# Kernel tuning notes

Measured on AMD Instinct MI355X. Metric: run time of the kernel, lower is better.

The kernel has to match this reference:

```python
import jax, jax.numpy as jnp
import numpy as np

B, C, H, W = 16, 256, 96, 96
PLANES = 64            # inplanes * ratio = 256 * 0.25
HEADS = 4
EPS = 1e-5             # BatchNorm eps


def setup_inputs() -> dict:
    key = jax.random.key(0)
    ks = jax.random.split(key, 8)
    HW = H * W
    G = HW // HEADS    # group size of the grouped 1x1 conv over spatial-positions-as-channels
    return {
        "x": jax.random.normal(ks[0], (B, C, H, W), jnp.float32),
        # input_conv: Conv1x1(C->PLANES) -> BN -> ReLU -> Conv1x1(PLANES->C)
        "w1": jax.random.normal(ks[1], (PLANES, C), jnp.float32) * (1.0 / np.sqrt(C)),
        "b1": jax.random.normal(ks[2], (PLANES,), jnp.float32) * 0.01,
        "gamma": jnp.ones((PLANES,), jnp.float32),
        "beta": jnp.zeros((PLANES,), jnp.float32),
        "mean": jnp.zeros((PLANES,), jnp.float32),
        "var": jnp.ones((PLANES,), jnp.float32),
        "w2": jax.random.normal(ks[3], (C, PLANES), jnp.float32) * (1.0 / np.sqrt(PLANES)),
        "b2": jax.random.normal(ks[4], (C,), jnp.float32) * 0.01,
        # conv_mask: Conv2d(HW, HEADS, k=1, groups=HEADS) -> weight [HEADS, G], bias [HEADS]
        "wm": jax.random.normal(ks[5], (HEADS, G), jnp.float32) * (1.0 / np.sqrt(G)),
        "bm": jax.random.normal(ks[6], (HEADS,), jnp.float32) * 0.01,
    }


def reference(x, w1, b1, gamma, beta, mean, var, w2, b2, wm, bm):
    Bx, Cx, Hx, Wx = x.shape
    G = (Hx * Wx) // HEADS
    # ---- input_conv: 1x1 conv -> BN (inference) -> ReLU -> 1x1 conv ----
    h = jnp.einsum('bchw,pc->bphw', x, w1) + b1[None, :, None, None]
    scale = (gamma / jnp.sqrt(var + EPS))[None, :, None, None]
    h = jax.nn.relu((h - mean[None, :, None, None]) * scale + beta[None, :, None, None])
    y = jnp.einsum('bphw,cp->bchw', h, w2) + b2[None, :, None, None]
    # ---- treat spatial positions as channels: [B, HEADS, G, C] ----
    ix = y.transpose(0, 2, 3, 1).reshape(Bx, HEADS, G, Cx)
    # grouped 1x1 conv over HW-channels -> logits [B, HEADS, C]
    logits = jnp.einsum('bhgc,hg->bhc', ix, wm) + bm[None, :, None]
    # softmax over channel axis (torch dim=2 of [B, HEADS, C, 1])
    mask = jax.nn.softmax(logits, axis=2)
    # context pooling matmul: [B,HEADS,G,C] @ [B,HEADS,C,1] -> [B,HEADS,G]
    ctx = jnp.einsum('bhgc,bhc->bhg', ix, mask)
    context = ctx.reshape(Bx, 1, Hx, Wx)
    # fusion_types = ('channel_add',)
    return x + context
```

## Files before the change

### kernel.cpp

```cpp
#include <hip/hip_runtime.h>

#define Bn 16
#define Cn 256
#define HWn 9216
#define Pn 64
#define HEADSn 4
#define Gn 2304
#define STILE 64
#define TILES_PER_B (HWn / STILE)
#define NTILE (Bn * TILES_PER_B)
#define T32_PER_B 288
#define NBLK1 (Bn * T32_PER_B)

typedef float f32x4 __attribute__((ext_vector_type(4)));
typedef short short4v __attribute__((ext_vector_type(4)));
typedef short short8 __attribute__((ext_vector_type(8)));
typedef unsigned int uint2v __attribute__((ext_vector_type(2)));

static __device__ __forceinline__ unsigned short f2bf(float f) {
    unsigned int b = __builtin_bit_cast(unsigned int, f);
    unsigned int r = b + 0x7FFFu + ((b >> 16) & 1u);
    return (unsigned short)(r >> 16);
}
static __device__ __forceinline__ float bf2f(unsigned short u) {
    unsigned int b = ((unsigned int)u) << 16;
    return __builtin_bit_cast(float, b);
}
static __device__ __forceinline__ unsigned int cvtpk(float a, float b) {
    unsigned int r;
    asm("v_cvt_pk_bf16_f32 %0, %1, %2" : "=v"(r) : "v"(a), "v"(b));
    return r;
}

__global__ __launch_bounds__(256)
void k0_prep(const float* __restrict__ w1, const float* __restrict__ b1,
             const float* __restrict__ gamma, const float* __restrict__ beta,
             const float* __restrict__ mean, const float* __restrict__ var,
             float* __restrict__ bcv, short* __restrict__ w1b)
{
    const int gid = blockIdx.x * 256 + threadIdx.x;
    if (gid < 2048) {
        const int row = gid >> 5;
        const float s = gamma[row] * rsqrtf(var[row] + 1e-5f);
        const float* p = w1 + gid * 8;
        short8 v;
        #pragma unroll
        for (int j = 0; j < 8; ++j) v[j] = (short)f2bf(p[j] * s);
        *reinterpret_cast<short8*>(&w1b[gid * 8]) = v;
    }
    if (gid < Pn) {
        const float s = gamma[gid] * rsqrtf(var[gid] + 1e-5f);
        bcv[gid] = (b1[gid] - mean[gid]) * s + beta[gid];
    }
}

__global__ __launch_bounds__(128, 4)
void k1_gemm(const float* __restrict__ x, const short* __restrict__ w1b,
             const float* __restrict__ bcv, const float* __restrict__ wm,
             float* __restrict__ hmp, short* __restrict__ hg)
{
    __shared__ short xl[Cn * 32];

    const int bid  = blockIdx.x;
    const int b    = bid / T32_PER_B;
    const int t32  = bid % T32_PER_B;
    const int s0   = t32 * 32;
    const int t    = threadIdx.x;
    const int lane = t & 63;
    const int wv   = t >> 6;
    const int g    = lane >> 4;
    const int m16  = lane & 15;

    short8 af[2][8];
    #pragma unroll
    for (int rt = 0; rt < 2; ++rt)
        #pragma unroll
        for (int ks = 0; ks < 8; ++ks)
            af[rt][ks] = *reinterpret_cast<const short8*>(
                w1b + (wv * 32 + rt * 16 + m16) * Cn + ks * 32 + g * 8);

    float bc[2][4];
    #pragma unroll
    for (int rt = 0; rt < 2; ++rt)
        #pragma unroll
        for (int r = 0; r < 4; ++r) bc[rt][r] = bcv[wv * 32 + rt * 16 + g * 4 + r];

    const int krow = t >> 3;
    const int chk  = t & 7;
    const float* xb = x + (size_t)b * Cn * HWn + s0 + chk * 4;
    #pragma unroll
    for (int i = 0; i < 16; ++i) {
        const int k = i * 16 + krow;
        const f32x4 v = *reinterpret_cast<const f32x4*>(xb + (size_t)k * HWn);
        uint2v pk;
        pk[0] = cvtpk(v[0], v[1]);
        pk[1] = cvtpk(v[2], v[3]);
        const int f    = (k ^ (k >> 2)) & 3;
        const int byte = k * 64 + (((chk >> 1) ^ f) * 16) + (chk & 1) * 8;
        *reinterpret_cast<uint2v*>(reinterpret_cast<char*>(xl) + byte) = pk;
    }
    __syncthreads();

    f32x4 acc[2][2] = { { {0,0,0,0}, {0,0,0,0} }, { {0,0,0,0}, {0,0,0,0} } };
    #pragma unroll
    for (int ks = 0; ks < 8; ++ks) {
        #pragma unroll
        for (int cg = 0; cg < 2; ++cg) {
            short8 bf;
            #pragma unroll
            for (int j = 0; j < 8; ++j) {
                const int k    = ks * 32 + g * 8 + j;
                const int f    = (k ^ (k >> 2)) & 3;
                const int byte = k * 64 + ((((cg * 2) + (m16 >> 3)) ^ f) * 16) + (m16 & 7) * 2;
                bf[j] = *reinterpret_cast<const short*>(
                    reinterpret_cast<const char*>(xl) + byte);
            }
            acc[cg][0] = __builtin_amdgcn_mfma_f32_16x16x32_bf16(af[0][ks], bf, acc[cg][0], 0, 0, 0);
            acc[cg][1] = __builtin_amdgcn_mfma_f32_16x16x32_bf16(af[1][ks], bf, acc[cg][1], 0, 0, 0);
        }
    }

    const float wmv0 = wm[s0 + m16];
    const float wmv1 = wm[s0 + 16 + m16];
    float hmacc[2][4];
    #pragma unroll
    for (int rt = 0; rt < 2; ++rt)
        #pragma unroll
        for (int r = 0; r < 4; ++r) hmacc[rt][r] = 0.f;

    #pragma unroll
    for (int cg = 0; cg < 2; ++cg) {
        const float wmv = cg ? wmv1 : wmv0;
        short* hrow = hg + ((size_t)b * HWn + s0 + cg * 16 + m16) * Pn + wv * 32;
        #pragma unroll
        for (int rt = 0; rt < 2; ++rt) {
            float h[4];
            #pragma unroll
            for (int r = 0; r < 4; ++r) {
                float hv = acc[cg][rt][r] + bc[rt][r];
                hv = hv > 0.f ? hv : 0.f;
                hmacc[rt][r] = fmaf(hv, wmv, hmacc[rt][r]);
                h[r] = hv;
            }
            uint2v pk;
            pk[0] = cvtpk(h[0], h[1]);
            pk[1] = cvtpk(h[2], h[3]);
            *reinterpret_cast<uint2v*>(hrow + rt * 16 + g * 4) = pk;
        }
    }

    #pragma unroll
    for (int rt = 0; rt < 2; ++rt)
        #pragma unroll
        for (int r = 0; r < 4; ++r) {
            float v = hmacc[rt][r];
            v += __shfl_xor(v, 1); v += __shfl_xor(v, 2);
            v += __shfl_xor(v, 4); v += __shfl_xor(v, 8);
            hmacc[rt][r] = v;
        }
    if (m16 == 0) {
        #pragma unroll
        for (int rt = 0; rt < 2; ++rt)
            #pragma unroll
            for (int r = 0; r < 4; ++r)
                hmp[bid * Pn + wv * 32 + rt * 16 + g * 4 + r] = hmacc[rt][r];
    }
}

__global__ __launch_bounds__(256)
void k2_mask(const float* __restrict__ hmp, const float* __restrict__ w2,
             const float* __restrict__ b2, const float* __restrict__ wm,
             float* __restrict__ wmix, float* __restrict__ bmix)
{
    __shared__ float hms[Pn];
    __shared__ float masks[Cn];
    __shared__ float red[4];
    __shared__ float part[4][Pn];

    const int bh = blockIdx.x;
    const int head = bh & (HEADSn - 1);
    const int t = threadIdx.x;
    const int l = t & 63;
    const int wv = t >> 6;

    {
        const int p = t & 63, q = t >> 6;
        const float* base = hmp + ((size_t)(bh >> 2) * T32_PER_B + head * 72) * Pn;
        float sp = 0.f;
        #pragma unroll
        for (int jj = 0; jj < 18; ++jj) sp += base[(q + 4 * jj) * Pn + p];
        part[q][p] = sp;
    }
    __syncthreads();
    if (t < Pn) hms[t] = part[0][t] + part[1][t] + part[2][t] + part[3][t];
    __syncthreads();

    float wsum = 0.f;
    for (int i = t; i < Gn; i += 256) wsum += wm[head * Gn + i];
    #pragma unroll
    for (int d = 1; d < 64; d <<= 1) wsum += __shfl_xor(wsum, d);
    if (l == 0) red[wv] = wsum;
    __syncthreads();
    wsum = red[0] + red[1] + red[2] + red[3];

    float lg = 0.f;
    #pragma unroll
    for (int k = 0; k < Pn; ++k) lg = fmaf(w2[t * Pn + k], hms[k], lg);
    lg = fmaf(b2[t], wsum, lg);

    float mx = lg;
    #pragma unroll
    for (int d = 1; d < 64; d <<= 1) mx = fmaxf(mx, __shfl_xor(mx, d));
    __syncthreads();
    if (l == 0) red[wv] = mx;
    __syncthreads();
    mx = fmaxf(fmaxf(red[0], red[1]), fmaxf(red[2], red[3]));
    const float ev = __expf(lg - mx);
    float sm = ev;
    #pragma unroll
    for (int d = 1; d < 64; d <<= 1) sm += __shfl_xor(sm, d);
    __syncthreads();
    if (l == 0) red[wv] = sm;
    __syncthreads();
    sm = red[0] + red[1] + red[2] + red[3];
    masks[t] = ev / sm;
    __syncthreads();

    {
        const int k = t & (Pn - 1);
        const int q = t >> 6;
        float wp = 0.f;
        #pragma unroll
        for (int i = 0; i < 64; ++i) {
            const int c = q * 64 + i;
            wp = fmaf(masks[c], w2[c * Pn + k], wp);
        }
        part[q][k] = wp;
    }
    __syncthreads();
    if (t < Pn) wmix[bh * Pn + t] = part[0][t] + part[1][t] + part[2][t] + part[3][t];

    float bp = masks[t] * b2[t];
    #pragma unroll
    for (int d = 1; d < 64; d <<= 1) bp += __shfl_xor(bp, d);
    __syncthreads();
    if (l == 0) red[wv] = bp;
    __syncthreads();
    if (t == 0) bmix[bh] = red[0] + red[1] + red[2] + red[3];
}

__global__ __launch_bounds__(256)
void k3_stream(const float* __restrict__ x, const short* __restrict__ hg,
               const float* __restrict__ wmix, const float* __restrict__ bmix,
               float* __restrict__ out)
{
    __shared__ float ctxl[STILE];

    const int bid  = blockIdx.x;
    const int b    = bid / TILES_PER_B;
    const int tile = bid % TILES_PER_B;
    const int s0   = tile * STILE;
    const int head = s0 / Gn;
    const int bh   = b * HEADSn + head;
    const int t    = threadIdx.x;

    if (t < STILE) {
        const short* hr = hg + ((size_t)b * HWn + s0 + t) * Pn;
        const float* wmx = wmix + bh * Pn;
        float acc = 0.f;
        #pragma unroll
        for (int i = 0; i < 8; ++i) {
            const short8 v = *reinterpret_cast<const short8*>(hr + i * 8);
            const f32x4 w0 = *reinterpret_cast<const f32x4*>(wmx + i * 8);
            const f32x4 w1v = *reinterpret_cast<const f32x4*>(wmx + i * 8 + 4);
            #pragma unroll
            for (int j = 0; j < 4; ++j) {
                acc = fmaf(bf2f((unsigned short)v[j]), w0[j], acc);
                acc = fmaf(bf2f((unsigned short)v[4 + j]), w1v[j], acc);
            }
        }
        ctxl[t] = acc + bmix[bh];
    }
    __syncthreads();

    const int c0 = t >> 4;
    const int s4 = t & 15;
    const f32x4 cv = *reinterpret_cast<const f32x4*>(&ctxl[s4 * 4]);
    const float* xb = x + (size_t)b * Cn * HWn + s0 + s4 * 4;
    float* ob = out + (size_t)b * Cn * HWn + s0 + s4 * 4;
    #pragma unroll
    for (int i = 0; i < 16; ++i) {
        const size_t off = (size_t)(c0 + 16 * i) * HWn;
        *reinterpret_cast<f32x4*>(ob + off) =
            *reinterpret_cast<const f32x4*>(xb + off) + cv;
    }
}

extern "C" void kernel_launch(void* const* d_in, const int* in_sizes, int n_in,
                              void* d_out, int out_size, void* d_ws, size_t ws_size,
                              hipStream_t stream)
{
    (void)in_sizes; (void)n_in; (void)out_size; (void)ws_size;
    const float* x     = (const float*)d_in[0];
    const float* w1    = (const float*)d_in[1];
    const float* b1    = (const float*)d_in[2];
    const float* gamma = (const float*)d_in[3];
    const float* beta  = (const float*)d_in[4];
    const float* mean  = (const float*)d_in[5];
    const float* var   = (const float*)d_in[6];
    const float* w2    = (const float*)d_in[7];
    const float* b2    = (const float*)d_in[8];
    const float* wm    = (const float*)d_in[9];

    float* out  = (float*)d_out;
    float* wsf  = (float*)d_ws;
    float* hmp  = wsf;
    float* wmix = hmp + NBLK1 * Pn;
    float* bmix = wmix + Bn * HEADSn * Pn;
    float* bcv  = bmix + 64;
    short* w1b  = (short*)(bcv + 64);
    short* hg   = w1b + Pn * Cn;

    k0_prep<<<dim3(8), dim3(256), 0, stream>>>(w1, b1, gamma, beta, mean, var, bcv, w1b);
    k1_gemm<<<dim3(NBLK1), dim3(128), 0, stream>>>(x, w1b, bcv, wm, hmp, hg);
    k2_mask<<<dim3(Bn * HEADSn), dim3(256), 0, stream>>>(hmp, w2, b2, wm, wmix, bmix);
    k3_stream<<<dim3(NTILE), dim3(256), 0, stream>>>(x, hg, wmix, bmix, out);
}
```

Measured before the change: 101.2 us.

## Split context computation into separate kernel and stream rows in final add

Moves the per-position context dot product (bf16 hidden × mixed weights) into its own kernel. That kernel uses 8 threads per position with a shuffle reduction and writes a per-batch context vector. The final streaming kernel now loads that context once and reuses it across 4 channel rows per block, reading and writing contiguous rows with full coalescing instead of 64-wide spatial tiles. This removes the serial 64-thread dot product and block barrier from the bandwidth-bound stream. The cost is an extra launch plus a small context buffer round-trip through global memory.

```diff
diff --git a/kernel.cpp b/kernel.cpp
--- a/kernel.cpp
+++ b/kernel.cpp
@@ -6,14 +6,10 @@
 #define Pn 64
 #define HEADSn 4
 #define Gn 2304
-#define STILE 64
-#define TILES_PER_B (HWn / STILE)
-#define NTILE (Bn * TILES_PER_B)
 #define T32_PER_B 288
 #define NBLK1 (Bn * T32_PER_B)
 
 typedef float f32x4 __attribute__((ext_vector_type(4)));
-typedef short short4v __attribute__((ext_vector_type(4)));
 typedef short short8 __attribute__((ext_vector_type(8)));
 typedef unsigned int uint2v __attribute__((ext_vector_type(2)));
 
@@ -250,49 +246,59 @@
 }
 
 __global__ __launch_bounds__(256)
-void k3_stream(const float* __restrict__ x, const short* __restrict__ hg,
-               const float* __restrict__ wmix, const float* __restrict__ bmix,
+void k2b_ctx(const short* __restrict__ hg, const float* __restrict__ wmix,
+             const float* __restrict__ bmix, float* __restrict__ ctxb)
+{
+    const int bid = blockIdx.x;
+    const int b   = bid / 288;
+    const int s32 = bid % 288;
+    const int head = s32 / 72;
+    const int bh  = b * HEADSn + head;
+    const int t   = threadIdx.x;
+    const int sr  = t >> 3;
+    const int j8  = t & 7;
+    const int s   = s32 * 32 + sr;
+
+    const short8 hv = *reinterpret_cast<const short8*>(
+        hg + ((size_t)b * HWn + s) * Pn + j8 * 8);
+    const f32x4 w0 = *reinterpret_cast<const f32x4*>(wmix + bh * Pn + j8 * 8);
+    const f32x4 w1v = *reinterpret_cast<const f32x4*>(wmix + bh * Pn + j8 * 8 + 4);
+    float acc = 0.f;
+    #pragma unroll
+    for (int j = 0; j < 4; ++j) {
+        acc = fmaf(bf2f((unsigned short)hv[j]), w0[j], acc);
+        acc = fmaf(bf2f((unsigned short)hv[4 + j]), w1v[j], acc);
+    }
+    acc += __shfl_xor(acc, 1);
+    acc += __shfl_xor(acc, 2);
+    acc += __shfl_xor(acc, 4);
+    if (j8 == 0) ctxb[(size_t)b * HWn + s] = acc + bmix[bh];
+}
+
+__global__ __launch_bounds__(256)
+void k3_stream(const float* __restrict__ x, const float* __restrict__ ctxb,
                float* __restrict__ out)
 {
-    __shared__ float ctxl[STILE];
-
-    const int bid  = blockIdx.x;
-    const int b    = bid / TILES_PER_B;
-    const int tile = bid % TILES_PER_B;
-    const int s0   = tile * STILE;
-    const int head = s0 / Gn;
-    const int bh   = b * HEADSn + head;
-    const int t    = threadIdx.x;
-
-    if (t < STILE) {
-        const short* hr = hg + ((size_t)b * HWn + s0 + t) * Pn;
-        const float* wmx = wmix + bh * Pn;
-        float acc = 0.f;
-        #pragma unroll
-        for (int i = 0; i < 8; ++i) {
-            const short8 v = *reinterpret_cast<const short8*>(hr + i * 8);
-            const f32x4 w0 = *reinterpret_cast<const f32x4*>(wmx + i * 8);
-            const f32x4 w1v = *reinterpret_cast<const f32x4*>(wmx + i * 8 + 4);
-            #pragma unroll
-            for (int j = 0; j < 4; ++j) {
-                acc = fmaf(bf2f((unsigned short)v[j]), w0[j], acc);
-                acc = fmaf(bf2f((unsigned short)v[4 + j]), w1v[j], acc);
-            }
-        }
-        ctxl[t] = acc + bmix[bh];
-    }
-    __syncthreads();
-
-    const int c0 = t >> 4;
-    const int s4 = t & 15;
-    const f32x4 cv = *reinterpret_cast<const f32x4*>(&ctxl[s4 * 4]);
-    const float* xb = x + (size_t)b * Cn * HWn + s0 + s4 * 4;
-    float* ob = out + (size_t)b * Cn * HWn + s0 + s4 * 4;
-    #pragma unroll
-    for (int i = 0; i < 16; ++i) {
-        const size_t off = (size_t)(c0 + 16 * i) * HWn;
-        *reinterpret_cast<f32x4*>(ob + off) =
-            *reinterpret_cast<const f32x4*>(xb + off) + cv;
+    const int bid = blockIdx.x;
+    const int b   = bid >> 6;
+    const int c0  = (bid & 63) * 4;
+    const int t   = threadIdx.x;
+
+    f32x4 cv[9];
+    #pragma unroll
+    for (int j = 0; j < 9; ++j)
+        cv[j] = *reinterpret_cast<const f32x4*>(ctxb + (size_t)b * HWn + (j * 256 + t) * 4);
+
+    #pragma unroll
+    for (int ci = 0; ci < 4; ++ci) {
+        const float* xr = x + ((size_t)b * Cn + c0 + ci) * HWn;
+        float* orow = out + ((size_t)b * Cn + c0 + ci) * HWn;
+        #pragma unroll
+        for (int j = 0; j < 9; ++j) {
+            const int off = (j * 256 + t) * 4;
+            *reinterpret_cast<f32x4*>(orow + off) =
+                *reinterpret_cast<const f32x4*>(xr + off) + cv[j];
+        }
     }
 }
 
@@ -318,11 +324,13 @@
     float* wmix = hmp + NBLK1 * Pn;
     float* bmix = wmix + Bn * HEADSn * Pn;
     float* bcv  = bmix + 64;
-    short* w1b  = (short*)(bcv + 64);
+    float* ctxb = bcv + 64;
+    short* w1b  = (short*)(ctxb + Bn * HWn);
     short* hg   = w1b + Pn * Cn;
 
     k0_prep<<<dim3(8), dim3(256), 0, stream>>>(w1, b1, gamma, beta, mean, var, bcv, w1b);
     k1_gemm<<<dim3(NBLK1), dim3(128), 0, stream>>>(x, w1b, bcv, wm, hmp, hg);
     k2_mask<<<dim3(Bn * HEADSn), dim3(256), 0, stream>>>(hmp, w2, b2, wm, wmix, bmix);
-    k3_stream<<<dim3(NTILE), dim3(256), 0, stream>>>(x, hg, wmix, bmix, out);
-}
+    k2b_ctx<<<dim3(Bn * 288), dim3(256), 0, stream>>>(hg, wmix, bmix, ctxb);
+    k3_stream<<<dim3(Bn * 64), dim3(256), 0, stream>>>(x, ctxb, out);
+}
```

Result: slower. 107.9 us (+6.6%).
